# Performance work log

Hardware: AMD Instinct MI355X
Metric: run time of the kernel (lower is better)

The kernel has to match this reference:

```python
import jax, jax.numpy as jnp
import numpy as np

NUM_EXPERTS = 8
TOP_K = 2
D = 1024


def setup_inputs() -> dict:
    key = jax.random.key(0)
    ks = jax.random.split(key, 5)
    T = 16384
    x = jax.random.normal(ks[0], (T, D), dtype=jnp.float32)
    # torch nn.Linear params: weight [out, in], bias [out]
    Wg = jax.random.normal(ks[1], (NUM_EXPERTS, D), dtype=jnp.float32) * (1.0 / np.sqrt(D))
    bg = jnp.zeros((NUM_EXPERTS,), dtype=jnp.float32)
    We = jax.random.normal(ks[2], (NUM_EXPERTS, D, D), dtype=jnp.float32) * (1.0 / np.sqrt(D))
    be = jax.random.normal(ks[3], (NUM_EXPERTS, D), dtype=jnp.float32) * 0.01
    return {"x": x, "Wg": Wg, "bg": bg, "We": We, "be": be}


def reference(x, Wg, bg, We, be):
    T = x.shape[0]
    # gate logits [T, E]
    gate_logits = x @ Wg.T + bg
    top_k_gates, top_k_idx = jax.lax.top_k(gate_logits, TOP_K)  # [T, K]
    top_k_gates = jax.nn.softmax(top_k_gates, axis=-1)
    # dense per-expert combine weight: sum of gate probs where idx == e
    combine = jnp.zeros((T, NUM_EXPERTS), dtype=x.dtype)
    combine = combine.at[jnp.arange(T)[:, None], top_k_idx].add(top_k_gates)  # [T, E]
    # all-expert dense matmul (faithful to the original naive loop): [E, T, out]
    expert_out = jnp.einsum('td,eod->eto', x, We) + be[:, None, :]
    # weighted combine: output[t] = sum_e combine[t,e] * expert_out[e,t]
    out = jnp.einsum('te,eto->to', combine, expert_out)
    return out
```

## Files before the change

### kernel.cpp

```cpp
#include <hip/hip_runtime.h>
#include <hip/hip_bf16.h>
#include <stdint.h>

#define DDIM 1024
#define NEXP 8
#define SEG  16384

typedef __attribute__((ext_vector_type(8))) short bf16x8;
typedef __attribute__((ext_vector_type(4))) float f32x4;
typedef __attribute__((ext_vector_type(8))) unsigned short u16x8;

__device__ __forceinline__ unsigned short f2bf(float f) {
    union { float f; unsigned int u; } v; v.f = f;
    unsigned int u = v.u;
    return (unsigned short)((u + 0x7FFFu + ((u >> 16) & 1u)) >> 16);
}
__device__ __forceinline__ float bf2f(unsigned short h) {
    union { unsigned int u; float f; } v; v.u = ((unsigned int)h) << 16;
    return v.f;
}

__global__ __launch_bounds__(512) void prep(
    const float* __restrict__ x, const float* __restrict__ Wg,
    const float* __restrict__ bg, const float* __restrict__ We,
    unsigned short* __restrict__ xb, unsigned short* __restrict__ web,
    int* __restrict__ cnt, int* __restrict__ tok_list,
    float* __restrict__ gate_list) {

    __shared__ int   se[64];
    __shared__ float sg[64];

    if (blockIdx.x >= 512) {
        size_t idx = ((size_t)(blockIdx.x - 512) * 512 + threadIdx.x) * 8;
        const f32x4* p = (const f32x4*)(We + idx);
        f32x4 a = __builtin_nontemporal_load(p);
        f32x4 b = __builtin_nontemporal_load(p + 1);
        u16x8 h;
        h[0] = f2bf(a[0]); h[1] = f2bf(a[1]); h[2] = f2bf(a[2]); h[3] = f2bf(a[3]);
        h[4] = f2bf(b[0]); h[5] = f2bf(b[1]); h[6] = f2bf(b[2]); h[7] = f2bf(b[3]);
        *(u16x8*)(web + idx) = h;
        return;
    }

    int wave = threadIdx.x >> 6, lane = threadIdx.x & 63;
    int tbase = blockIdx.x * 32;

#pragma unroll
    for (int i = 0; i < 4; i++) {
        int lt = wave * 4 + i;
        int t = tbase + lt;
        const float* xr = x + (size_t)t * DDIM;
        int c0 = lane * 8;

        float4 v0 = ((const float4*)(xr + c0))[0];
        float4 v1 = ((const float4*)(xr + c0))[1];
        float4 v2 = ((const float4*)(xr + c0 + 512))[0];
        float4 v3 = ((const float4*)(xr + c0 + 512))[1];

        u16x8 h0, h1;
        h0[0] = f2bf(v0.x); h0[1] = f2bf(v0.y); h0[2] = f2bf(v0.z); h0[3] = f2bf(v0.w);
        h0[4] = f2bf(v1.x); h0[5] = f2bf(v1.y); h0[6] = f2bf(v1.z); h0[7] = f2bf(v1.w);
        h1[0] = f2bf(v2.x); h1[1] = f2bf(v2.y); h1[2] = f2bf(v2.z); h1[3] = f2bf(v2.w);
        h1[4] = f2bf(v3.x); h1[5] = f2bf(v3.y); h1[6] = f2bf(v3.z); h1[7] = f2bf(v3.w);
        *(u16x8*)(xb + (size_t)t * DDIM + c0) = h0;
        *(u16x8*)(xb + (size_t)t * DDIM + c0 + 512) = h1;

        float acc[NEXP];
#pragma unroll
        for (int e = 0; e < NEXP; e++) {
            const float* wr = Wg + e * DDIM;
            float4 w0 = ((const float4*)(wr + c0))[0];
            float4 w1 = ((const float4*)(wr + c0))[1];
            float4 w2 = ((const float4*)(wr + c0 + 512))[0];
            float4 w3 = ((const float4*)(wr + c0 + 512))[1];
            float s = v0.x*w0.x + v0.y*w0.y + v0.z*w0.z + v0.w*w0.w;
            s += v1.x*w1.x + v1.y*w1.y + v1.z*w1.z + v1.w*w1.w;
            s += v2.x*w2.x + v2.y*w2.y + v2.z*w2.z + v2.w*w2.w;
            s += v3.x*w3.x + v3.y*w3.y + v3.z*w3.z + v3.w*w3.w;
            acc[e] = s;
        }
#pragma unroll
        for (int e = 0; e < NEXP; e++) {
#pragma unroll
            for (int o = 32; o > 0; o >>= 1) acc[e] += __shfl_xor(acc[e], o, 64);
        }

        if (lane == 0) {
            float l1 = -1e30f, l2 = -1e30f; int e1 = 0, e2 = 0;
#pragma unroll
            for (int e = 0; e < NEXP; e++) {
                float le = acc[e] + bg[e];
                if (le > l1) { l2 = l1; e2 = e1; l1 = le; e1 = e; }
                else if (le > l2) { l2 = le; e2 = e; }
            }
            float g1 = 1.0f / (1.0f + __expf(l2 - l1));
            float g2 = 1.0f - g1;
            se[lt * 2]     = e1; sg[lt * 2]     = g1;
            se[lt * 2 + 1] = e2; sg[lt * 2 + 1] = g2;
        }
    }
    __syncthreads();

    if (threadIdx.x < NEXP) {
        int e = threadIdx.x;
        int k = 0;
#pragma unroll 8
        for (int i = 0; i < 64; i++) k += (se[i] == e);
        if (k) {
            int p = atomicAdd(cnt + e, k);
            for (int i = 0; i < 64; i++) {
                if (se[i] == e) {
                    tok_list[e * SEG + p]  = (tbase + (i >> 1)) * 2 + (i & 1);
                    gate_list[e * SEG + p] = sg[i];
                    p++;
                }
            }
        }
    }
}


__device__ __forceinline__ void stage_tile(const unsigned short* const* sp,
                                           unsigned short* lbase, int wave, int kt) {
    int ko = kt << 5;
#pragma unroll
    for (int j = 0; j < 6; ++j) {
        __builtin_amdgcn_global_load_lds(
            (const __attribute__((address_space(1))) void*)(sp[j] + ko),
            (__attribute__((address_space(3))) void*)(lbase + (wave * 6 + j) * 512),
            16, 0, 0);
    }
}

__device__ __forceinline__ void tile_mma(const unsigned short* ba, int aoff, int boff,
                                         f32x4 (&acc)[8][4]) {
    bf16x8 af[8], bf[4];
#pragma unroll
    for (int mi = 0; mi < 8; ++mi) af[mi] = *(const bf16x8*)(ba + aoff + mi * 512);
#pragma unroll
    for (int ni = 0; ni < 4; ++ni) bf[ni] = *(const bf16x8*)(ba + boff + ni * 512);
    __builtin_amdgcn_s_setprio(1);
#pragma unroll
    for (int mi = 0; mi < 8; ++mi)
#pragma unroll
        for (int ni = 0; ni < 4; ++ni)
            acc[mi][ni] = __builtin_amdgcn_mfma_f32_16x16x32_bf16(
                af[mi], bf[ni], acc[mi][ni], 0, 0, 0);
    __builtin_amdgcn_s_setprio(0);
}

template<bool STORE>
__global__ __launch_bounds__(256, 2) void moe_gemm(
    const unsigned short* __restrict__ xb, const unsigned short* __restrict__ web,
    const float* __restrict__ be, const int* __restrict__ cnt,
    const int* __restrict__ tok_list, const float* __restrict__ gate_list,
    unsigned short* __restrict__ Sb, float* __restrict__ outa) {

    extern __shared__ __align__(16) unsigned short lbuf[];
    __shared__ int   tok_s[128];
    __shared__ float gate_s[128];

    int id = blockIdx.y, e = 0, c = 0;
    while (e < NEXP) {
        c = cnt[e];
        int mt = (c + 127) >> 7;
        if (id < mt) break;
        id -= mt; e++;
    }
    if (e == NEXP) return;
    int m0 = id << 7;
    int n0 = blockIdx.x << 8;

    int tid = threadIdx.x;
    int wave = tid >> 6, lane = tid & 63;

    if (tid < 128) {
        int r = m0 + tid;
        int rc = min(r, c - 1);
        tok_s[tid]  = tok_list[e * SEG + rc];
        gate_s[tid] = (r < c) ? gate_list[e * SEG + rc] : 0.0f;
    }
    __syncthreads();

    int g0 = ((lane & 3) - ((lane >> 3) & 3)) & 3;
    const unsigned short* sp[6];
#pragma unroll
    for (int j = 0; j < 6; ++j) {
        int ch = wave * 6 + j;
        int sub = lane >> 2;
        int arow = min((ch << 4) + sub, 127);
        int brow = ((ch - 8) << 4) + sub;
        const unsigned short* pa = xb + (size_t)(tok_s[arow] >> 1) * DDIM + g0 * 8;
        const unsigned short* pb = web + ((size_t)e << 20) +
                                   (size_t)(n0 + brow) * DDIM + g0 * 8;
        sp[j] = (ch < 8) ? pa : pb;
    }

    int mrow = lane & 15, q = lane >> 4;
    int ksl  = ((q + (mrow >> 1)) & 3) << 3;
    int aoff = mrow * 32 + ksl;
    int boff = 4096 + wave * 2048 + mrow * 32 + ksl;

    f32x4 acc[8][4];
    f32x4 zz = {0.f, 0.f, 0.f, 0.f};
#pragma unroll
    for (int mi = 0; mi < 8; ++mi)
#pragma unroll
        for (int ni = 0; ni < 4; ++ni) acc[mi][ni] = zz;

    stage_tile(sp, lbuf,         wave, 0);
    stage_tile(sp, lbuf + 12288, wave, 1);

    for (int kb = 0; kb < 10; ++kb) {
#pragma unroll
        for (int u = 0; u < 3; ++u) {
            int kt = kb * 3 + u;
            asm volatile("s_waitcnt vmcnt(6)" ::: "memory");
            __builtin_amdgcn_s_barrier();
            asm volatile("" ::: "memory");
            stage_tile(sp, lbuf + ((u + 2) % 3) * 12288, wave, kt + 2);
            tile_mma(lbuf + u * 12288, aoff, boff, acc);
        }
    }
    asm volatile("s_waitcnt vmcnt(6)" ::: "memory");
    __builtin_amdgcn_s_barrier();
    asm volatile("" ::: "memory");
    tile_mma(lbuf, aoff, boff, acc);

    asm volatile("s_waitcnt vmcnt(0)" ::: "memory");
    __builtin_amdgcn_s_barrier();
    asm volatile("" ::: "memory");
    tile_mma(lbuf + 12288, aoff, boff, acc);

    if (STORE) {
        __syncthreads();
#pragma unroll
        for (int ni = 0; ni < 4; ++ni) {
            int col = wave * 64 + ni * 16 + mrow;
            float bias = be[e * DDIM + n0 + col];
            int cg = col >> 3, cl = col & 7;
#pragma unroll
            for (int mi = 0; mi < 8; ++mi) {
#pragma unroll
                for (int r = 0; r < 4; ++r) {
                    int row = mi * 16 + q * 4 + r;
                    float vv = gate_s[row] * (acc[mi][ni][r] + bias);
                    lbuf[row * 256 + ((cg ^ (row & 7)) << 3) + cl] = f2bf(vv);
                }
            }
        }
        __syncthreads();
#pragma unroll
        for (int j = 0; j < 16; ++j) {
            int t = j * 256 + tid;
            int row = t >> 5, gc = t & 31;
            u16x8 vv = *(const u16x8*)&lbuf[row * 256 + ((gc ^ (row & 7)) << 3)];
            if (m0 + row < c)
                *(u16x8*)(Sb + (size_t)tok_s[row] * DDIM + n0 + gc * 8) = vv;
        }
    } else {
#pragma unroll
        for (int ni = 0; ni < 4; ++ni) {
            int col = n0 + wave * 64 + ni * 16 + mrow;
            float bias = be[e * DDIM + col];
#pragma unroll
            for (int mi = 0; mi < 8; ++mi) {
#pragma unroll
                for (int r = 0; r < 4; ++r) {
                    int rl = mi * 16 + q * 4 + r;
                    if (m0 + rl < c)
                        atomicAdd(outa + (size_t)(tok_s[rl] >> 1) * DDIM + col,
                                  gate_s[rl] * (acc[mi][ni][r] + bias));
                }
            }
        }
    }
}

__global__ void combine(const unsigned short* __restrict__ S, float* __restrict__ out) {
    size_t i = (size_t)blockIdx.x * 256 + threadIdx.x;
    size_t t = i >> 7;
    size_t g = i & 127;
    const u16x8* r0 = (const u16x8*)(S + t * 2 * DDIM) + g;
    const u16x8* r1 = (const u16x8*)(S + (t * 2 + 1) * DDIM) + g;
    u16x8 a = *r0;
    u16x8 b = *r1;
    f32x4 o0, o1;
#pragma unroll
    for (int k = 0; k < 4; k++) o0[k] = bf2f(a[k]) + bf2f(b[k]);
#pragma unroll
    for (int k = 0; k < 4; k++) o1[k] = bf2f(a[4 + k]) + bf2f(b[4 + k]);
    f32x4* op = (f32x4*)(out + t * DDIM + g * 8);
    __builtin_nontemporal_store(o0, op);
    __builtin_nontemporal_store(o1, op + 1);
}

extern "C" void kernel_launch(void* const* d_in, const int* in_sizes, int n_in,
                              void* d_out, int out_size, void* d_ws, size_t ws_size,
                              hipStream_t stream) {
    const float* x  = (const float*)d_in[0];
    const float* Wg = (const float*)d_in[1];
    const float* bg = (const float*)d_in[2];
    const float* We = (const float*)d_in[3];
    const float* be = (const float*)d_in[4];
    float* out = (float*)d_out;

    char* ws = (char*)d_ws;
    unsigned short* xb  = (unsigned short*)ws;
    unsigned short* web = (unsigned short*)(ws + 33554432);
    int*   tok_list  = (int*)(ws + 33554432 + 16777216);
    float* gate_list = (float*)(ws + 33554432 + 16777216 + 524288);
    int*   cnt       = (int*)(ws + 33554432 + 16777216 + 1048576);
    unsigned short* S = (unsigned short*)(ws + 52428800);

    const size_t NEED = 52428800ull + (size_t)32768 * DDIM * 2;

    static bool attr_done = false;
    if (!attr_done) {
        hipFuncSetAttribute(reinterpret_cast<const void*>(moe_gemm<true>),
                            hipFuncAttributeMaxDynamicSharedMemorySize, 73728);
        hipFuncSetAttribute(reinterpret_cast<const void*>(moe_gemm<false>),
                            hipFuncAttributeMaxDynamicSharedMemorySize, 73728);
        attr_done = true;
    }

    hipMemsetAsync(cnt, 0, NEXP * sizeof(int), stream);

    prep<<<2560, 512, 0, stream>>>(x, Wg, bg, We, xb, web, cnt, tok_list, gate_list);

    if (ws_size >= NEED) {
        moe_gemm<true><<<dim3(4, 264), 256, 73728, stream>>>(
            xb, web, be, cnt, tok_list, gate_list, S, nullptr);
        combine<<<8192, 256, 0, stream>>>(S, out);
    } else {
        hipMemsetAsync(d_out, 0, (size_t)out_size * sizeof(float), stream);
        moe_gemm<false><<<dim3(4, 264), 256, 73728, stream>>>(
            xb, web, be, cnt, tok_list, gate_list, nullptr, out);
    }
}
```

Baseline: 276.6 us.

## Rewrite MoE GEMM as persistent 256x256-tile kernel with 8 waves and double buffering

Replaces the 128x256 tile, 4-wave GEMM grid with a persistent kernel of 256 blocks of 512 threads. Each block pulls 256x256 output tiles from an atomic work counter. The K loop uses 64-wide double-buffered LDS stages with loads interleaved between MFMA sub-phases, and the XOR-swizzled layout is rebuilt for the larger tile. The goal is more data reuse per LDS byte, better latency hiding and less tail imbalance. In exchange it uses 128KB of LDS per block, many more barriers, and an unswizzled epilogue store that may cause LDS bank conflicts.

```diff
diff --git a/kernel.cpp b/kernel.cpp
--- a/kernel.cpp
+++ b/kernel.cpp
@@ -9,6 +9,9 @@
 typedef __attribute__((ext_vector_type(8))) short bf16x8;
 typedef __attribute__((ext_vector_type(4))) float f32x4;
 typedef __attribute__((ext_vector_type(8))) unsigned short u16x8;
+
+#define AS1 __attribute__((address_space(1)))
+#define AS3 __attribute__((address_space(3)))
 
 __device__ __forceinline__ unsigned short f2bf(float f) {
     union { float f; unsigned int u; } v; v.f = f;
@@ -120,157 +123,210 @@
 }
 
 
-__device__ __forceinline__ void stage_tile(const unsigned short* const* sp,
-                                           unsigned short* lbase, int wave, int kt) {
-    int ko = kt << 5;
-#pragma unroll
-    for (int j = 0; j < 6; ++j) {
-        __builtin_amdgcn_global_load_lds(
-            (const __attribute__((address_space(1))) void*)(sp[j] + ko),
-            (__attribute__((address_space(3))) void*)(lbase + (wave * 6 + j) * 512),
-            16, 0, 0);
-    }
-}
-
-__device__ __forceinline__ void tile_mma(const unsigned short* ba, int aoff, int boff,
-                                         f32x4 (&acc)[8][4]) {
-    bf16x8 af[8], bf[4];
-#pragma unroll
-    for (int mi = 0; mi < 8; ++mi) af[mi] = *(const bf16x8*)(ba + aoff + mi * 512);
-#pragma unroll
-    for (int ni = 0; ni < 4; ++ni) bf[ni] = *(const bf16x8*)(ba + boff + ni * 512);
-    __builtin_amdgcn_s_setprio(1);
-#pragma unroll
-    for (int mi = 0; mi < 8; ++mi)
-#pragma unroll
-        for (int ni = 0; ni < 4; ++ni)
-            acc[mi][ni] = __builtin_amdgcn_mfma_f32_16x16x32_bf16(
-                af[mi], bf[ni], acc[mi][ni], 0, 0, 0);
-    __builtin_amdgcn_s_setprio(0);
-}
+#define STAGE(P0_, P1_, DSTOFF_, KO_) do {                                     \
+    __builtin_amdgcn_global_load_lds((const AS1 void*)((P0_) + (KO_)),         \
+        (AS3 void*)(lbuf + (DSTOFF_)), 16, 0, 0);                              \
+    __builtin_amdgcn_global_load_lds((const AS1 void*)((P1_) + (KO_)),         \
+        (AS3 void*)(lbuf + (DSTOFF_) + 512), 16, 0, 0);                        \
+} while (0)
 
 template<bool STORE>
-__global__ __launch_bounds__(256, 2) void moe_gemm(
+__global__ __launch_bounds__(512, 2) void moe_gemm(
     const unsigned short* __restrict__ xb, const unsigned short* __restrict__ web,
     const float* __restrict__ be, const int* __restrict__ cnt,
     const int* __restrict__ tok_list, const float* __restrict__ gate_list,
-    unsigned short* __restrict__ Sb, float* __restrict__ outa) {
+    unsigned short* __restrict__ Sb, float* __restrict__ outa,
+    int* __restrict__ wctr) {
 
     extern __shared__ __align__(16) unsigned short lbuf[];
-    __shared__ int   tok_s[128];
-    __shared__ float gate_s[128];
-
-    int id = blockIdx.y, e = 0, c = 0;
-    while (e < NEXP) {
-        c = cnt[e];
-        int mt = (c + 127) >> 7;
-        if (id < mt) break;
-        id -= mt; e++;
-    }
-    if (e == NEXP) return;
-    int m0 = id << 7;
-    int n0 = blockIdx.x << 8;
+    __shared__ int   tok_s[256];
+    __shared__ float gate_s[256];
+    __shared__ int   s_id;
 
     int tid = threadIdx.x;
-    int wave = tid >> 6, lane = tid & 63;
-
-    if (tid < 128) {
-        int r = m0 + tid;
-        int rc = min(r, c - 1);
-        tok_s[tid]  = tok_list[e * SEG + rc];
-        gate_s[tid] = (r < c) ? gate_list[e * SEG + rc] : 0.0f;
-    }
-    __syncthreads();
-
-    int g0 = ((lane & 3) - ((lane >> 3) & 3)) & 3;
-    const unsigned short* sp[6];
-#pragma unroll
-    for (int j = 0; j < 6; ++j) {
-        int ch = wave * 6 + j;
-        int sub = lane >> 2;
-        int arow = min((ch << 4) + sub, 127);
-        int brow = ((ch - 8) << 4) + sub;
-        const unsigned short* pa = xb + (size_t)(tok_s[arow] >> 1) * DDIM + g0 * 8;
-        const unsigned short* pb = web + ((size_t)e << 20) +
-                                   (size_t)(n0 + brow) * DDIM + g0 * 8;
-        sp[j] = (ch < 8) ? pa : pb;
-    }
-
+    int w = tid >> 6, lane = tid & 63;
+    int wave_m = w >> 2, wave_n = w & 3;
     int mrow = lane & 15, q = lane >> 4;
-    int ksl  = ((q + (mrow >> 1)) & 3) << 3;
-    int aoff = mrow * 32 + ksl;
-    int boff = 4096 + wave * 2048 + mrow * 32 + ksl;
-
-    f32x4 acc[8][4];
-    f32x4 zz = {0.f, 0.f, 0.f, 0.f};
-#pragma unroll
-    for (int mi = 0; mi < 8; ++mi)
-#pragma unroll
-        for (int ni = 0; ni < 4; ++ni) acc[mi][ni] = zz;
-
-    stage_tile(sp, lbuf,         wave, 0);
-    stage_tile(sp, lbuf + 12288, wave, 1);
-
-    for (int kb = 0; kb < 10; ++kb) {
-#pragma unroll
-        for (int u = 0; u < 3; ++u) {
-            int kt = kb * 3 + u;
-            asm volatile("s_waitcnt vmcnt(6)" ::: "memory");
-            __builtin_amdgcn_s_barrier();
-            asm volatile("" ::: "memory");
-            stage_tile(sp, lbuf + ((u + 2) % 3) * 12288, wave, kt + 2);
-            tile_mma(lbuf + u * 12288, aoff, boff, acc);
-        }
-    }
-    asm volatile("s_waitcnt vmcnt(6)" ::: "memory");
-    __builtin_amdgcn_s_barrier();
-    asm volatile("" ::: "memory");
-    tile_mma(lbuf, aoff, boff, acc);
-
-    asm volatile("s_waitcnt vmcnt(0)" ::: "memory");
-    __builtin_amdgcn_s_barrier();
-    asm volatile("" ::: "memory");
-    tile_mma(lbuf + 12288, aoff, boff, acc);
-
-    if (STORE) {
+    int m7 = mrow & 7;
+    int s0 = (q + m7) & 7;
+    int s1 = s0 ^ 4;
+    int aBase = (wave_m * 128 + mrow) * 64;
+    int bBase = 16384 + (wave_n * 64 + mrow) * 64;
+    int gsrc = ((lane & 7) - (lane >> 3)) & 7;
+    int sub8 = lane >> 3;
+
+    for (;;) {
+        if (tid == 0) s_id = atomicAdd(wctr, 1);
         __syncthreads();
-#pragma unroll
-        for (int ni = 0; ni < 4; ++ni) {
-            int col = wave * 64 + ni * 16 + mrow;
-            float bias = be[e * DDIM + n0 + col];
-            int cg = col >> 3, cl = col & 7;
-#pragma unroll
-            for (int mi = 0; mi < 8; ++mi) {
-#pragma unroll
-                for (int r = 0; r < 4; ++r) {
-                    int row = mi * 16 + q * 4 + r;
-                    float vv = gate_s[row] * (acc[mi][ni][r] + bias);
-                    lbuf[row * 256 + ((cg ^ (row & 7)) << 3) + cl] = f2bf(vv);
+        int id = s_id;
+        int e = 0, c = 0, rem = id;
+        while (e < NEXP) {
+            c = cnt[e];
+            int t_e = ((c + 255) >> 8) << 2;
+            if (rem < t_e) break;
+            rem -= t_e; e++;
+        }
+        if (e == NEXP) return;
+        int m0 = (rem >> 2) << 8;
+        int n0 = (rem & 3) << 8;
+
+        if (tid < 256) {
+            int r = m0 + tid;
+            int rc = min(r, c - 1);
+            tok_s[tid]  = tok_list[e * SEG + rc];
+            gate_s[tid] = (r < c) ? gate_list[e * SEG + rc] : 0.0f;
+        }
+        __syncthreads();
+
+        const unsigned short* pA[2][2];
+        const unsigned short* pB[2][2];
+#pragma unroll
+        for (int h = 0; h < 2; ++h)
+#pragma unroll
+            for (int j = 0; j < 2; ++j) {
+                int row = h * 128 + w * 16 + j * 8 + sub8;
+                pA[h][j] = xb + (size_t)(tok_s[row] >> 1) * DDIM + gsrc * 8;
+                pB[h][j] = web + ((size_t)e << 20) + (size_t)(n0 + row) * DDIM + gsrc * 8;
+            }
+
+        f32x4 acc[8][4];
+#pragma unroll
+        for (int mi = 0; mi < 8; ++mi)
+#pragma unroll
+            for (int ni = 0; ni < 4; ++ni) acc[mi][ni] = (f32x4){0.f, 0.f, 0.f, 0.f};
+
+        STAGE(pB[0][0], pB[0][1], 16384 + w * 1024, 0);
+        STAGE(pB[1][0], pB[1][1], 16384 + 8192 + w * 1024, 0);
+        STAGE(pA[0][0], pA[0][1], 0 + w * 1024, 0);
+        STAGE(pA[1][0], pA[1][1], 8192 + w * 1024, 0);
+        STAGE(pB[0][0], pB[0][1], 32768 + 16384 + w * 1024, 64);
+        STAGE(pB[1][0], pB[1][1], 32768 + 16384 + 8192 + w * 1024, 64);
+        STAGE(pA[0][0], pA[0][1], 32768 + 0 + w * 1024, 64);
+
+#pragma unroll 2
+        for (int kt = 0; kt < 16; ++kt) {
+            if (kt == 15) { asm volatile("s_waitcnt vmcnt(0)" ::: "memory"); }
+            else          { asm volatile("s_waitcnt vmcnt(6)" ::: "memory"); }
+            __builtin_amdgcn_s_barrier();
+
+            int bufo = (kt & 1) << 15;
+            int nb   = ((kt + 1) & 1) << 15;
+            int ko1  = (kt + 1) << 6;
+            int ko2  = (kt + 2) << 6;
+
+            bf16x8 B0[4], B1[4], A0[4], A1[4];
+
+#pragma unroll
+            for (int ni = 0; ni < 4; ++ni)
+                B0[ni] = *(const bf16x8*)(lbuf + bufo + bBase + ni * 1024 + s0 * 8);
+#pragma unroll
+            for (int ni = 0; ni < 4; ++ni)
+                B1[ni] = *(const bf16x8*)(lbuf + bufo + bBase + ni * 1024 + s1 * 8);
+#pragma unroll
+            for (int mi = 0; mi < 4; ++mi)
+                A0[mi] = *(const bf16x8*)(lbuf + bufo + aBase + mi * 1024 + s0 * 8);
+            if (kt < 15) STAGE(pA[1][0], pA[1][1], nb + 8192 + w * 1024, ko1);
+            __builtin_amdgcn_s_barrier();
+            asm volatile("s_waitcnt lgkmcnt(0)" ::: "memory");
+            __builtin_amdgcn_sched_barrier(0);
+            __builtin_amdgcn_s_setprio(1);
+#pragma unroll
+            for (int mi = 0; mi < 4; ++mi)
+#pragma unroll
+                for (int ni = 0; ni < 4; ++ni)
+                    acc[mi][ni] = __builtin_amdgcn_mfma_f32_16x16x32_bf16(
+                        A0[mi], B0[ni], acc[mi][ni], 0, 0, 0);
+            __builtin_amdgcn_s_setprio(0);
+            __builtin_amdgcn_s_barrier();
+
+#pragma unroll
+            for (int mi = 0; mi < 4; ++mi)
+                A1[mi] = *(const bf16x8*)(lbuf + bufo + aBase + (mi + 4) * 1024 + s0 * 8);
+            if (kt < 14) STAGE(pB[0][0], pB[0][1], bufo + 16384 + w * 1024, ko2);
+            __builtin_amdgcn_s_barrier();
+            asm volatile("s_waitcnt lgkmcnt(0)" ::: "memory");
+            __builtin_amdgcn_sched_barrier(0);
+            __builtin_amdgcn_s_setprio(1);
+#pragma unroll
+            for (int mi = 0; mi < 4; ++mi)
+#pragma unroll
+                for (int ni = 0; ni < 4; ++ni)
+                    acc[mi + 4][ni] = __builtin_amdgcn_mfma_f32_16x16x32_bf16(
+                        A1[mi], B0[ni], acc[mi + 4][ni], 0, 0, 0);
+            __builtin_amdgcn_s_setprio(0);
+            __builtin_amdgcn_s_barrier();
+
+#pragma unroll
+            for (int mi = 0; mi < 4; ++mi)
+                A0[mi] = *(const bf16x8*)(lbuf + bufo + aBase + mi * 1024 + s1 * 8);
+#pragma unroll
+            for (int mi = 0; mi < 4; ++mi)
+                A1[mi] = *(const bf16x8*)(lbuf + bufo + aBase + (mi + 4) * 1024 + s1 * 8);
+            if (kt < 14) STAGE(pB[1][0], pB[1][1], bufo + 16384 + 8192 + w * 1024, ko2);
+            __builtin_amdgcn_s_barrier();
+            asm volatile("s_waitcnt lgkmcnt(0)" ::: "memory");
+            __builtin_amdgcn_sched_barrier(0);
+            __builtin_amdgcn_s_setprio(1);
+#pragma unroll
+            for (int mi = 0; mi < 4; ++mi)
+#pragma unroll
+                for (int ni = 0; ni < 4; ++ni)
+                    acc[mi][ni] = __builtin_amdgcn_mfma_f32_16x16x32_bf16(
+                        A0[mi], B1[ni], acc[mi][ni], 0, 0, 0);
+            __builtin_amdgcn_s_setprio(0);
+            __builtin_amdgcn_s_barrier();
+
+            if (kt < 14) STAGE(pA[0][0], pA[0][1], bufo + w * 1024, ko2);
+            __builtin_amdgcn_s_barrier();
+            __builtin_amdgcn_s_setprio(1);
+#pragma unroll
+            for (int mi = 0; mi < 4; ++mi)
+#pragma unroll
+                for (int ni = 0; ni < 4; ++ni)
+                    acc[mi + 4][ni] = __builtin_amdgcn_mfma_f32_16x16x32_bf16(
+                        A1[mi], B1[ni], acc[mi + 4][ni], 0, 0, 0);
+            __builtin_amdgcn_s_setprio(0);
+        }
+
+        if (STORE) {
+            __syncthreads();
+#pragma unroll
+            for (int ni = 0; ni < 4; ++ni) {
+                int col = wave_n * 64 + ni * 16 + mrow;
+                float bias = be[e * DDIM + n0 + col];
+#pragma unroll
+                for (int mi = 0; mi < 8; ++mi) {
+#pragma unroll
+                    for (int r = 0; r < 4; ++r) {
+                        int row = wave_m * 128 + mi * 16 + q * 4 + r;
+                        lbuf[row * 256 + col] = f2bf(gate_s[row] * (acc[mi][ni][r] + bias));
+                    }
                 }
             }
-        }
-        __syncthreads();
-#pragma unroll
-        for (int j = 0; j < 16; ++j) {
-            int t = j * 256 + tid;
-            int row = t >> 5, gc = t & 31;
-            u16x8 vv = *(const u16x8*)&lbuf[row * 256 + ((gc ^ (row & 7)) << 3)];
-            if (m0 + row < c)
-                *(u16x8*)(Sb + (size_t)tok_s[row] * DDIM + n0 + gc * 8) = vv;
-        }
-    } else {
-#pragma unroll
-        for (int ni = 0; ni < 4; ++ni) {
-            int col = n0 + wave * 64 + ni * 16 + mrow;
-            float bias = be[e * DDIM + col];
-#pragma unroll
-            for (int mi = 0; mi < 8; ++mi) {
-#pragma unroll
-                for (int r = 0; r < 4; ++r) {
-                    int rl = mi * 16 + q * 4 + r;
-                    if (m0 + rl < c)
-                        atomicAdd(outa + (size_t)(tok_s[rl] >> 1) * DDIM + col,
-                                  gate_s[rl] * (acc[mi][ni][r] + bias));
+            __syncthreads();
+#pragma unroll
+            for (int j = 0; j < 16; ++j) {
+                int t = j * 512 + tid;
+                int row = t >> 5, gc = t & 31;
+                u16x8 vv = *(const u16x8*)&lbuf[row * 256 + gc * 8];
+                if (m0 + row < c)
+                    *(u16x8*)(Sb + (size_t)tok_s[row] * DDIM + n0 + gc * 8) = vv;
+            }
+        } else {
+            __syncthreads();
+#pragma unroll
+            for (int ni = 0; ni < 4; ++ni) {
+                int col = n0 + wave_n * 64 + ni * 16 + mrow;
+                float bias = be[e * DDIM + col];
+#pragma unroll
+                for (int mi = 0; mi < 8; ++mi) {
+#pragma unroll
+                    for (int r = 0; r < 4; ++r) {
+                        int rl = wave_m * 128 + mi * 16 + q * 4 + r;
+                        if (m0 + rl < c)
+                            atomicAdd(outa + (size_t)(tok_s[rl] >> 1) * DDIM + col,
+                                      gate_s[rl] * (acc[mi][ni][r] + bias));
+                    }
                 }
             }
         }
@@ -313,28 +369,30 @@
     int*   cnt       = (int*)(ws + 33554432 + 16777216 + 1048576);
     unsigned short* S = (unsigned short*)(ws + 52428800);
 
+    int* wctr = cnt + NEXP;
+
     const size_t NEED = 52428800ull + (size_t)32768 * DDIM * 2;
 
     static bool attr_done = false;
     if (!attr_done) {
         hipFuncSetAttribute(reinterpret_cast<const void*>(moe_gemm<true>),
-                            hipFuncAttributeMaxDynamicSharedMemorySize, 73728);
+                            hipFuncAttributeMaxDynamicSharedMemorySize, 131072);
         hipFuncSetAttribute(reinterpret_cast<const void*>(moe_gemm<false>),
-                            hipFuncAttributeMaxDynamicSharedMemorySize, 73728);
+                            hipFuncAttributeMaxDynamicSharedMemorySize, 131072);
         attr_done = true;
     }
 
-    hipMemsetAsync(cnt, 0, NEXP * sizeof(int), stream);
+    hipMemsetAsync(cnt, 0, (NEXP + 1) * sizeof(int), stream);
 
     prep<<<2560, 512, 0, stream>>>(x, Wg, bg, We, xb, web, cnt, tok_list, gate_list);
 
     if (ws_size >= NEED) {
-        moe_gemm<true><<<dim3(4, 264), 256, 73728, stream>>>(
-            xb, web, be, cnt, tok_list, gate_list, S, nullptr);
+        moe_gemm<true><<<256, 512, 131072, stream>>>(
+            xb, web, be, cnt, tok_list, gate_list, S, nullptr, wctr);
         combine<<<8192, 256, 0, stream>>>(S, out);
     } else {
         hipMemsetAsync(d_out, 0, (size_t)out_size * sizeof(float), stream);
-        moe_gemm<false><<<dim3(4, 264), 256, 73728, stream>>>(
-            xb, web, be, cnt, tok_list, gate_list, nullptr, out);
-    }
-}
+        moe_gemm<false><<<256, 512, 131072, stream>>>(
+            xb, web, be, cnt, tok_list, gate_list, nullptr, out, wctr);
+    }
+}
```

Result: slower. 340.8 us (+23.2%).

## Convert MoE grouped GEMM to persistent blocks with atomic work counter

Applied to the files above, without the earlier changes.

Replaces the fixed 4x264 grid, in which many blocks exit early, with 512 persistent blocks. Each block repeatedly grabs a tile index from a global atomic counter and decodes it into expert, row tile and column tile. This removes launch and idle-block overhead and balances the tail across CUs. In exchange it adds an atomic and an extra block-wide sync per tile, and tiles from the same expert are no longer guaranteed to run at the same time.

```diff
diff --git a/kernel.cpp b/kernel.cpp
--- a/kernel.cpp
+++ b/kernel.cpp
@@ -9,6 +9,9 @@
 typedef __attribute__((ext_vector_type(8))) short bf16x8;
 typedef __attribute__((ext_vector_type(4))) float f32x4;
 typedef __attribute__((ext_vector_type(8))) unsigned short u16x8;
+
+#define AS1 __attribute__((address_space(1)))
+#define AS3 __attribute__((address_space(3)))
 
 __device__ __forceinline__ unsigned short f2bf(float f) {
     union { float f; unsigned int u; } v; v.f = f;
@@ -126,8 +129,8 @@
 #pragma unroll
     for (int j = 0; j < 6; ++j) {
         __builtin_amdgcn_global_load_lds(
-            (const __attribute__((address_space(1))) void*)(sp[j] + ko),
-            (__attribute__((address_space(3))) void*)(lbase + (wave * 6 + j) * 512),
+            (const AS1 void*)(sp[j] + ko),
+            (AS3 void*)(lbase + (wave * 6 + j) * 512),
             16, 0, 0);
     }
 }
@@ -154,123 +157,130 @@
     const unsigned short* __restrict__ xb, const unsigned short* __restrict__ web,
     const float* __restrict__ be, const int* __restrict__ cnt,
     const int* __restrict__ tok_list, const float* __restrict__ gate_list,
-    unsigned short* __restrict__ Sb, float* __restrict__ outa) {
+    unsigned short* __restrict__ Sb, float* __restrict__ outa,
+    int* __restrict__ wctr) {
 
     extern __shared__ __align__(16) unsigned short lbuf[];
     __shared__ int   tok_s[128];
     __shared__ float gate_s[128];
-
-    int id = blockIdx.y, e = 0, c = 0;
-    while (e < NEXP) {
-        c = cnt[e];
-        int mt = (c + 127) >> 7;
-        if (id < mt) break;
-        id -= mt; e++;
-    }
-    if (e == NEXP) return;
-    int m0 = id << 7;
-    int n0 = blockIdx.x << 8;
+    __shared__ int   s_id;
 
     int tid = threadIdx.x;
     int wave = tid >> 6, lane = tid & 63;
-
-    if (tid < 128) {
-        int r = m0 + tid;
-        int rc = min(r, c - 1);
-        tok_s[tid]  = tok_list[e * SEG + rc];
-        gate_s[tid] = (r < c) ? gate_list[e * SEG + rc] : 0.0f;
-    }
-    __syncthreads();
-
-    int g0 = ((lane & 3) - ((lane >> 3) & 3)) & 3;
-    const unsigned short* sp[6];
-#pragma unroll
-    for (int j = 0; j < 6; ++j) {
-        int ch = wave * 6 + j;
-        int sub = lane >> 2;
-        int arow = min((ch << 4) + sub, 127);
-        int brow = ((ch - 8) << 4) + sub;
-        const unsigned short* pa = xb + (size_t)(tok_s[arow] >> 1) * DDIM + g0 * 8;
-        const unsigned short* pb = web + ((size_t)e << 20) +
-                                   (size_t)(n0 + brow) * DDIM + g0 * 8;
-        sp[j] = (ch < 8) ? pa : pb;
-    }
 
     int mrow = lane & 15, q = lane >> 4;
     int ksl  = ((q + (mrow >> 1)) & 3) << 3;
     int aoff = mrow * 32 + ksl;
     int boff = 4096 + wave * 2048 + mrow * 32 + ksl;
-
-    f32x4 acc[8][4];
-    f32x4 zz = {0.f, 0.f, 0.f, 0.f};
-#pragma unroll
-    for (int mi = 0; mi < 8; ++mi)
-#pragma unroll
-        for (int ni = 0; ni < 4; ++ni) acc[mi][ni] = zz;
-
-    stage_tile(sp, lbuf,         wave, 0);
-    stage_tile(sp, lbuf + 12288, wave, 1);
-
-    for (int kb = 0; kb < 10; ++kb) {
-#pragma unroll
-        for (int u = 0; u < 3; ++u) {
-            int kt = kb * 3 + u;
-            asm volatile("s_waitcnt vmcnt(6)" ::: "memory");
-            __builtin_amdgcn_s_barrier();
-            asm volatile("" ::: "memory");
-            stage_tile(sp, lbuf + ((u + 2) % 3) * 12288, wave, kt + 2);
-            tile_mma(lbuf + u * 12288, aoff, boff, acc);
-        }
-    }
-    asm volatile("s_waitcnt vmcnt(6)" ::: "memory");
-    __builtin_amdgcn_s_barrier();
-    asm volatile("" ::: "memory");
-    tile_mma(lbuf, aoff, boff, acc);
-
-    asm volatile("s_waitcnt vmcnt(0)" ::: "memory");
-    __builtin_amdgcn_s_barrier();
-    asm volatile("" ::: "memory");
-    tile_mma(lbuf + 12288, aoff, boff, acc);
-
-    if (STORE) {
+    int g0  = ((lane & 3) - ((lane >> 3) & 3)) & 3;
+    int sub = lane >> 2;
+
+    for (;;) {
+        if (tid == 0) s_id = atomicAdd(wctr, 1);
         __syncthreads();
-#pragma unroll
-        for (int ni = 0; ni < 4; ++ni) {
-            int col = wave * 64 + ni * 16 + mrow;
-            float bias = be[e * DDIM + n0 + col];
-            int cg = col >> 3, cl = col & 7;
-#pragma unroll
-            for (int mi = 0; mi < 8; ++mi) {
-#pragma unroll
-                for (int r = 0; r < 4; ++r) {
-                    int row = mi * 16 + q * 4 + r;
-                    float vv = gate_s[row] * (acc[mi][ni][r] + bias);
-                    lbuf[row * 256 + ((cg ^ (row & 7)) << 3) + cl] = f2bf(vv);
+        int id = s_id;
+        int e = 0, c = 0, rem = id;
+        while (e < NEXP) {
+            c = cnt[e];
+            int t_e = ((c + 127) >> 7) << 2;
+            if (rem < t_e) break;
+            rem -= t_e; e++;
+        }
+        if (e == NEXP) return;
+        int m0 = (rem >> 2) << 7;
+        int n0 = (rem & 3) << 8;
+
+        if (tid < 128) {
+            int r = m0 + tid;
+            int rc = min(r, c - 1);
+            tok_s[tid]  = tok_list[e * SEG + rc];
+            gate_s[tid] = (r < c) ? gate_list[e * SEG + rc] : 0.0f;
+        }
+        __syncthreads();
+
+        const unsigned short* sp[6];
+#pragma unroll
+        for (int j = 0; j < 6; ++j) {
+            int ch = wave * 6 + j;
+            int arow = min((ch << 4) + sub, 127);
+            int brow = ((ch - 8) << 4) + sub;
+            const unsigned short* pa = xb + (size_t)(tok_s[arow] >> 1) * DDIM + g0 * 8;
+            const unsigned short* pb = web + ((size_t)e << 20) +
+                                       (size_t)(n0 + brow) * DDIM + g0 * 8;
+            sp[j] = (ch < 8) ? pa : pb;
+        }
+
+        f32x4 acc[8][4];
+#pragma unroll
+        for (int mi = 0; mi < 8; ++mi)
+#pragma unroll
+            for (int ni = 0; ni < 4; ++ni) acc[mi][ni] = (f32x4){0.f, 0.f, 0.f, 0.f};
+
+        stage_tile(sp, lbuf,         wave, 0);
+        stage_tile(sp, lbuf + 12288, wave, 1);
+
+        for (int kb = 0; kb < 10; ++kb) {
+#pragma unroll
+            for (int u = 0; u < 3; ++u) {
+                int kt = kb * 3 + u;
+                asm volatile("s_waitcnt vmcnt(6)" ::: "memory");
+                __builtin_amdgcn_s_barrier();
+                asm volatile("" ::: "memory");
+                stage_tile(sp, lbuf + ((u + 2) % 3) * 12288, wave, kt + 2);
+                tile_mma(lbuf + u * 12288, aoff, boff, acc);
+            }
+        }
+        asm volatile("s_waitcnt vmcnt(6)" ::: "memory");
+        __builtin_amdgcn_s_barrier();
+        asm volatile("" ::: "memory");
+        tile_mma(lbuf, aoff, boff, acc);
+
+        asm volatile("s_waitcnt vmcnt(0)" ::: "memory");
+        __builtin_amdgcn_s_barrier();
+        asm volatile("" ::: "memory");
+        tile_mma(lbuf + 12288, aoff, boff, acc);
+
+        if (STORE) {
+            __syncthreads();
+#pragma unroll
+            for (int ni = 0; ni < 4; ++ni) {
+                int col = wave * 64 + ni * 16 + mrow;
+                float bias = be[e * DDIM + n0 + col];
+                int cg = col >> 3, cl = col & 7;
+#pragma unroll
+                for (int mi = 0; mi < 8; ++mi) {
+#pragma unroll
+                    for (int r = 0; r < 4; ++r) {
+                        int row = mi * 16 + q * 4 + r;
+                        lbuf[row * 256 + ((cg ^ (row & 7)) << 3) + cl] =
+                            f2bf(gate_s[row] * (acc[mi][ni][r] + bias));
+                    }
                 }
             }
-        }
-        __syncthreads();
-#pragma unroll
-        for (int j = 0; j < 16; ++j) {
-            int t = j * 256 + tid;
-            int row = t >> 5, gc = t & 31;
-            u16x8 vv = *(const u16x8*)&lbuf[row * 256 + ((gc ^ (row & 7)) << 3)];
-            if (m0 + row < c)
-                *(u16x8*)(Sb + (size_t)tok_s[row] * DDIM + n0 + gc * 8) = vv;
-        }
-    } else {
-#pragma unroll
-        for (int ni = 0; ni < 4; ++ni) {
-            int col = n0 + wave * 64 + ni * 16 + mrow;
-            float bias = be[e * DDIM + col];
-#pragma unroll
-            for (int mi = 0; mi < 8; ++mi) {
-#pragma unroll
-                for (int r = 0; r < 4; ++r) {
-                    int rl = mi * 16 + q * 4 + r;
-                    if (m0 + rl < c)
-                        atomicAdd(outa + (size_t)(tok_s[rl] >> 1) * DDIM + col,
-                                  gate_s[rl] * (acc[mi][ni][r] + bias));
+            __syncthreads();
+#pragma unroll
+            for (int j = 0; j < 16; ++j) {
+                int t = j * 256 + tid;
+                int row = t >> 5, gc = t & 31;
+                u16x8 vv = *(const u16x8*)&lbuf[row * 256 + ((gc ^ (row & 7)) << 3)];
+                if (m0 + row < c)
+                    *(u16x8*)(Sb + (size_t)tok_s[row] * DDIM + n0 + gc * 8) = vv;
+            }
+        } else {
+            __syncthreads();
+#pragma unroll
+            for (int ni = 0; ni < 4; ++ni) {
+                int col = n0 + wave * 64 + ni * 16 + mrow;
+                float bias = be[e * DDIM + col];
+#pragma unroll
+                for (int mi = 0; mi < 8; ++mi) {
+#pragma unroll
+                    for (int r = 0; r < 4; ++r) {
+                        int rl = mi * 16 + q * 4 + r;
+                        if (m0 + rl < c)
+                            atomicAdd(outa + (size_t)(tok_s[rl] >> 1) * DDIM + col,
+                                      gate_s[rl] * (acc[mi][ni][r] + bias));
+                    }
                 }
             }
         }
@@ -313,6 +323,8 @@
     int*   cnt       = (int*)(ws + 33554432 + 16777216 + 1048576);
     unsigned short* S = (unsigned short*)(ws + 52428800);
 
+    int* wctr = cnt + NEXP;
+
     const size_t NEED = 52428800ull + (size_t)32768 * DDIM * 2;
 
     static bool attr_done = false;
@@ -324,17 +336,17 @@
         attr_done = true;
     }
 
-    hipMemsetAsync(cnt, 0, NEXP * sizeof(int), stream);
+    hipMemsetAsync(cnt, 0, (NEXP + 1) * sizeof(int), stream);
 
     prep<<<2560, 512, 0, stream>>>(x, Wg, bg, We, xb, web, cnt, tok_list, gate_list);
 
     if (ws_size >= NEED) {
-        moe_gemm<true><<<dim3(4, 264), 256, 73728, stream>>>(
-            xb, web, be, cnt, tok_list, gate_list, S, nullptr);
+        moe_gemm<true><<<512, 256, 73728, stream>>>(
+            xb, web, be, cnt, tok_list, gate_list, S, nullptr, wctr);
         combine<<<8192, 256, 0, stream>>>(S, out);
     } else {
         hipMemsetAsync(d_out, 0, (size_t)out_size * sizeof(float), stream);
-        moe_gemm<false><<<dim3(4, 264), 256, 73728, stream>>>(
-            xb, web, be, cnt, tok_list, gate_list, nullptr, out);
-    }
-}
+        moe_gemm<false><<<512, 256, 73728, stream>>>(
+            xb, web, be, cnt, tok_list, gate_list, nullptr, out, wctr);
+    }
+}
```

Result: slower. 375.3 us (+35.7%).

## Split MoE GEMM block into 8 waves with 2x4 wave grid

Applied to the files above, without the earlier changes.

Doubles the moe_gemm workgroup from 4 to 8 waves, arranging them as a 2x4 grid so each wave computes a 64x64 sub-tile instead of 128x64. Each wave now stages 3 LDS chunks instead of 6 and holds half the accumulators, cutting register pressure and raising the number of resident waves for latency hiding. In exchange, the ratio of LDS reads to MFMA issues per wave rises (A fragments are shared across fewer columns), and barriers now synchronise more waves.

```diff
diff --git a/kernel.cpp b/kernel.cpp
--- a/kernel.cpp
+++ b/kernel.cpp
@@ -9,6 +9,9 @@
 typedef __attribute__((ext_vector_type(8))) short bf16x8;
 typedef __attribute__((ext_vector_type(4))) float f32x4;
 typedef __attribute__((ext_vector_type(8))) unsigned short u16x8;
+
+#define AS1 __attribute__((address_space(1)))
+#define AS3 __attribute__((address_space(3)))
 
 __device__ __forceinline__ unsigned short f2bf(float f) {
     union { float f; unsigned int u; } v; v.f = f;
@@ -124,24 +127,24 @@
                                            unsigned short* lbase, int wave, int kt) {
     int ko = kt << 5;
 #pragma unroll
-    for (int j = 0; j < 6; ++j) {
+    for (int j = 0; j < 3; ++j) {
         __builtin_amdgcn_global_load_lds(
-            (const __attribute__((address_space(1))) void*)(sp[j] + ko),
-            (__attribute__((address_space(3))) void*)(lbase + (wave * 6 + j) * 512),
+            (const AS1 void*)(sp[j] + ko),
+            (AS3 void*)(lbase + (wave * 3 + j) * 512),
             16, 0, 0);
     }
 }
 
 __device__ __forceinline__ void tile_mma(const unsigned short* ba, int aoff, int boff,
-                                         f32x4 (&acc)[8][4]) {
-    bf16x8 af[8], bf[4];
-#pragma unroll
-    for (int mi = 0; mi < 8; ++mi) af[mi] = *(const bf16x8*)(ba + aoff + mi * 512);
+                                         f32x4 (&acc)[4][4]) {
+    bf16x8 af[4], bf[4];
+#pragma unroll
+    for (int mi = 0; mi < 4; ++mi) af[mi] = *(const bf16x8*)(ba + aoff + mi * 512);
 #pragma unroll
     for (int ni = 0; ni < 4; ++ni) bf[ni] = *(const bf16x8*)(ba + boff + ni * 512);
     __builtin_amdgcn_s_setprio(1);
 #pragma unroll
-    for (int mi = 0; mi < 8; ++mi)
+    for (int mi = 0; mi < 4; ++mi)
 #pragma unroll
         for (int ni = 0; ni < 4; ++ni)
             acc[mi][ni] = __builtin_amdgcn_mfma_f32_16x16x32_bf16(
@@ -150,7 +153,7 @@
 }
 
 template<bool STORE>
-__global__ __launch_bounds__(256, 2) void moe_gemm(
+__global__ __launch_bounds__(512, 2) void moe_gemm(
     const unsigned short* __restrict__ xb, const unsigned short* __restrict__ web,
     const float* __restrict__ be, const int* __restrict__ cnt,
     const int* __restrict__ tok_list, const float* __restrict__ gate_list,
@@ -172,7 +175,8 @@
     int n0 = blockIdx.x << 8;
 
     int tid = threadIdx.x;
-    int wave = tid >> 6, lane = tid & 63;
+    int w = tid >> 6, lane = tid & 63;
+    int wave_m = w >> 2, wave_n = w & 3;
 
     if (tid < 128) {
         int r = m0 + tid;
@@ -182,12 +186,17 @@
     }
     __syncthreads();
 
-    int g0 = ((lane & 3) - ((lane >> 3) & 3)) & 3;
-    const unsigned short* sp[6];
-#pragma unroll
-    for (int j = 0; j < 6; ++j) {
-        int ch = wave * 6 + j;
-        int sub = lane >> 2;
+    int mrow = lane & 15, q = lane >> 4;
+    int ksl  = ((q + (mrow >> 1)) & 3) << 3;
+    int aoff = (wave_m * 64 + mrow) * 32 + ksl;
+    int boff = 4096 + (wave_n * 64 + mrow) * 32 + ksl;
+
+    int g0  = ((lane & 3) - ((lane >> 3) & 3)) & 3;
+    int sub = lane >> 2;
+    const unsigned short* sp[3];
+#pragma unroll
+    for (int j = 0; j < 3; ++j) {
+        int ch = w * 3 + j;
         int arow = min((ch << 4) + sub, 127);
         int brow = ((ch - 8) << 4) + sub;
         const unsigned short* pa = xb + (size_t)(tok_s[arow] >> 1) * DDIM + g0 * 8;
@@ -196,33 +205,27 @@
         sp[j] = (ch < 8) ? pa : pb;
     }
 
-    int mrow = lane & 15, q = lane >> 4;
-    int ksl  = ((q + (mrow >> 1)) & 3) << 3;
-    int aoff = mrow * 32 + ksl;
-    int boff = 4096 + wave * 2048 + mrow * 32 + ksl;
-
-    f32x4 acc[8][4];
-    f32x4 zz = {0.f, 0.f, 0.f, 0.f};
-#pragma unroll
-    for (int mi = 0; mi < 8; ++mi)
-#pragma unroll
-        for (int ni = 0; ni < 4; ++ni) acc[mi][ni] = zz;
-
-    stage_tile(sp, lbuf,         wave, 0);
-    stage_tile(sp, lbuf + 12288, wave, 1);
+    f32x4 acc[4][4];
+#pragma unroll
+    for (int mi = 0; mi < 4; ++mi)
+#pragma unroll
+        for (int ni = 0; ni < 4; ++ni) acc[mi][ni] = (f32x4){0.f, 0.f, 0.f, 0.f};
+
+    stage_tile(sp, lbuf,         w, 0);
+    stage_tile(sp, lbuf + 12288, w, 1);
 
     for (int kb = 0; kb < 10; ++kb) {
 #pragma unroll
         for (int u = 0; u < 3; ++u) {
             int kt = kb * 3 + u;
-            asm volatile("s_waitcnt vmcnt(6)" ::: "memory");
+            asm volatile("s_waitcnt vmcnt(3)" ::: "memory");
             __builtin_amdgcn_s_barrier();
             asm volatile("" ::: "memory");
-            stage_tile(sp, lbuf + ((u + 2) % 3) * 12288, wave, kt + 2);
+            stage_tile(sp, lbuf + ((u + 2) % 3) * 12288, w, kt + 2);
             tile_mma(lbuf + u * 12288, aoff, boff, acc);
         }
     }
-    asm volatile("s_waitcnt vmcnt(6)" ::: "memory");
+    asm volatile("s_waitcnt vmcnt(3)" ::: "memory");
     __builtin_amdgcn_s_barrier();
     asm volatile("" ::: "memory");
     tile_mma(lbuf, aoff, boff, acc);
@@ -236,38 +239,39 @@
         __syncthreads();
 #pragma unroll
         for (int ni = 0; ni < 4; ++ni) {
-            int col = wave * 64 + ni * 16 + mrow;
+            int col = wave_n * 64 + ni * 16 + mrow;
             float bias = be[e * DDIM + n0 + col];
             int cg = col >> 3, cl = col & 7;
 #pragma unroll
-            for (int mi = 0; mi < 8; ++mi) {
+            for (int mi = 0; mi < 4; ++mi) {
 #pragma unroll
                 for (int r = 0; r < 4; ++r) {
-                    int row = mi * 16 + q * 4 + r;
-                    float vv = gate_s[row] * (acc[mi][ni][r] + bias);
-                    lbuf[row * 256 + ((cg ^ (row & 7)) << 3) + cl] = f2bf(vv);
+                    int row = wave_m * 64 + mi * 16 + q * 4 + r;
+                    lbuf[row * 256 + ((cg ^ (row & 7)) << 3) + cl] =
+                        f2bf(gate_s[row] * (acc[mi][ni][r] + bias));
                 }
             }
         }
         __syncthreads();
 #pragma unroll
-        for (int j = 0; j < 16; ++j) {
-            int t = j * 256 + tid;
+        for (int j = 0; j < 8; ++j) {
+            int t = j * 512 + tid;
             int row = t >> 5, gc = t & 31;
             u16x8 vv = *(const u16x8*)&lbuf[row * 256 + ((gc ^ (row & 7)) << 3)];
             if (m0 + row < c)
                 *(u16x8*)(Sb + (size_t)tok_s[row] * DDIM + n0 + gc * 8) = vv;
         }
     } else {
+        __syncthreads();
 #pragma unroll
         for (int ni = 0; ni < 4; ++ni) {
-            int col = n0 + wave * 64 + ni * 16 + mrow;
+            int col = n0 + wave_n * 64 + ni * 16 + mrow;
             float bias = be[e * DDIM + col];
 #pragma unroll
-            for (int mi = 0; mi < 8; ++mi) {
+            for (int mi = 0; mi < 4; ++mi) {
 #pragma unroll
                 for (int r = 0; r < 4; ++r) {
-                    int rl = mi * 16 + q * 4 + r;
+                    int rl = wave_m * 64 + mi * 16 + q * 4 + r;
                     if (m0 + rl < c)
                         atomicAdd(outa + (size_t)(tok_s[rl] >> 1) * DDIM + col,
                                   gate_s[rl] * (acc[mi][ni][r] + bias));
@@ -329,12 +333,12 @@
     prep<<<2560, 512, 0, stream>>>(x, Wg, bg, We, xb, web, cnt, tok_list, gate_list);
 
     if (ws_size >= NEED) {
-        moe_gemm<true><<<dim3(4, 264), 256, 73728, stream>>>(
+        moe_gemm<true><<<dim3(4, 264), 512, 73728, stream>>>(
             xb, web, be, cnt, tok_list, gate_list, S, nullptr);
         combine<<<8192, 256, 0, stream>>>(S, out);
     } else {
         hipMemsetAsync(d_out, 0, (size_t)out_size * sizeof(float), stream);
-        moe_gemm<false><<<dim3(4, 264), 256, 73728, stream>>>(
+        moe_gemm<false><<<dim3(4, 264), 512, 73728, stream>>>(
             xb, web, be, cnt, tok_list, gate_list, nullptr, out);
     }
 }
```

After: 272.5 us. About the same (-1.5%).
